# Kernel optimization log

Hardware: AMD Instinct MI355X
Metric: run time of the kernel (lower is better)

## Reference

```python
import jax, jax.numpy as jnp
import numpy as np

H = 768; NH = 12; HD = 64; LW = 256
NEG = -1e9  # finite stand-in for -inf; exp underflows to 0 identically in fp32 softmax

def setup_inputs() -> dict:
    key = jax.random.key(0)
    ks = jax.random.split(key, 10)
    s = 0.02
    return {
        "x": jax.random.normal(ks[0], (2, 2048, H), dtype=jnp.float32),
        "w_attn": jax.random.normal(ks[1], (H, 3 * H), dtype=jnp.float32) * s,
        "b_attn": jnp.zeros((3 * H,), dtype=jnp.float32),
        "w_proj": jax.random.normal(ks[2], (H, H), dtype=jnp.float32) * s,
        "b_proj": jnp.zeros((H,), dtype=jnp.float32),
        "w_sel1": jax.random.normal(ks[3], (H, H // 4), dtype=jnp.float32) * s,
        "b_sel1": jnp.zeros((H // 4,), dtype=jnp.float32),
        "w_sel2": jax.random.normal(ks[4], (H // 4, 1), dtype=jnp.float32) * s,
        "b_sel2": jnp.zeros((1,), dtype=jnp.float32),
        "local_weight": jnp.float32(0.5),
        "global_weight": jnp.float32(0.5),
    }

def reference(x, w_attn, b_attn, w_proj, b_proj, w_sel1, b_sel1, w_sel2, b_sel2,
              local_weight, global_weight):
    B, T, C = x.shape
    scale = HD ** -0.5
    qkv = x @ w_attn + b_attn                       # [B,T,3C]
    q, k, v = jnp.split(qkv, 3, axis=-1)
    q = q.reshape(B, T, NH, HD).transpose(0, 2, 1, 3)  # [B,H,T,D]
    k = k.reshape(B, T, NH, HD).transpose(0, 2, 1, 3)
    v = v.reshape(B, T, NH, HD).transpose(0, 2, 1, 3)
    scores = jnp.einsum('bhqd,bhkd->bhqk', q, k) * scale  # [B,H,T,T]
    i = jnp.arange(T)[:, None]
    j = jnp.arange(T)[None, :]
    causal = j > i
    scores = jnp.where(causal[None, None], NEG, scores)
    # selectivity: per-key-position gate in [0.2, 1.0]
    sel = jax.nn.sigmoid(jax.nn.gelu(x @ w_sel1 + b_sel1, approximate=False) @ w_sel2 + b_sel2)  # [B,T,1]
    sel = sel[:, None, :, 0][:, :, None, :]            # [B,1,1,T]
    modulated = scores * (0.2 + 0.8 * sel)
    outside_local = j < jnp.clip(i - LW, 0, None)
    local = jnp.where(outside_local[None, None], NEG, scores)
    wl = jax.nn.sigmoid(local_weight)
    wg = jax.nn.sigmoid(global_weight)
    wsum = wl + wg
    wl, wg = wl / wsum, wg / wsum
    attn = wl * jax.nn.softmax(local, axis=-1) + wg * jax.nn.softmax(modulated, axis=-1)
    out = jnp.einsum('bhqk,bhkd->bhqd', attn, v)        # [B,H,T,D]
    out = out.transpose(0, 2, 1, 3).reshape(B, T, C)
    return out @ w_proj + b_proj
```

## Files before the change

kernel.cpp:

```cpp
#include <hip/hip_runtime.h>
#include <cmath>

#define TT    2048
#define CC    768
#define NHEAD 12
#define LWIN  256
#define BBATCH 2
#define MROWS 4096
#define QBA   128
#define KB    64
#define NSLOT 72
#define L2E   1.4426950408889634f

typedef unsigned int u32;
typedef u32 u32x2 __attribute__((ext_vector_type(2)));
typedef u32 u32x4 __attribute__((ext_vector_type(4)));
typedef short bf16x8 __attribute__((ext_vector_type(8)));
typedef float f32x16 __attribute__((ext_vector_type(16)));

union F4 { u32x4 u; bf16x8 h; };

__device__ __forceinline__ unsigned short b16(float a) {
  u32 u = __float_as_uint(a);
  return (unsigned short)((u + 0x7FFFu + ((u >> 16) & 1u)) >> 16);
}
__device__ __forceinline__ u32 pk2(float a, float b) {
  return (u32)b16(a) | ((u32)b16(b) << 16);
}

__global__ __launch_bounds__(256) void cvt_bf16_kernel(
    const float* __restrict__ in, unsigned short* __restrict__ out, int n8) {
  const int i = blockIdx.x * 256 + threadIdx.x;
  if (i >= n8) return;
  const float4 a = *(const float4*)&in[(size_t)i * 8];
  const float4 b = *(const float4*)&in[(size_t)i * 8 + 4];
  u32x4 w = {pk2(a.x, a.y), pk2(a.z, a.w), pk2(b.x, b.y), pk2(b.z, b.w)};
  *(u32x4*)&out[(size_t)i * 8] = w;
}

__global__ __launch_bounds__(256) void transpose_cvt_kernel(
    const float* __restrict__ W, unsigned short* __restrict__ Wt, int K, int N) {
  __shared__ float t[32][33];
  const int tid = threadIdx.x;
  const int n0 = blockIdx.x * 32, k0 = blockIdx.y * 32;
  const int r = tid >> 5, c = tid & 31;
#pragma unroll
  for (int rr = 0; rr < 4; ++rr)
    t[r + 8 * rr][c] = W[(size_t)(k0 + r + 8 * rr) * N + n0 + c];
  __syncthreads();
#pragma unroll
  for (int rr = 0; rr < 4; ++rr)
    Wt[(size_t)(n0 + r + 8 * rr) * K + k0 + c] = b16(t[c][r + 8 * rr]);
}

template <int NT, bool OUTBF, int ACT>
__global__ __launch_bounds__(256) void gemm_mfma_kernel(
    const unsigned short* __restrict__ A, const unsigned short* __restrict__ Bt,
    const float* __restrict__ bias, void* __restrict__ Cout,
    int M, int N, int K) {
  __shared__ alignas(16) unsigned short as_[128 * 64];
  __shared__ alignas(16) unsigned short bs_[NT * 32 * 64];
  const int tid = threadIdx.x;
  const int lane = tid & 63;
  const int wv = tid >> 6;
  const int hi = lane >> 5;
  const int l31 = lane & 31;
  const int m0 = blockIdx.y * 128, n0 = blockIdx.x * (NT * 32);

  u32x4 ar[4], br[NT];

#define G_ISSUE(K0)                                                           \
  do {                                                                        \
    _Pragma("unroll") for (int i = 0; i < 4; ++i) {                           \
      const int idx = tid + (i << 8);                                         \
      const int r = idx >> 3, c = idx & 7;                                    \
      ar[i] = *(const u32x4*)&A[(size_t)(m0 + r) * K + (K0) + c * 8];         \
    }                                                                         \
    _Pragma("unroll") for (int i = 0; i < NT; ++i) {                          \
      const int idx = tid + (i << 8);                                         \
      const int r = idx >> 3, c = idx & 7;                                    \
      br[i] = *(const u32x4*)&Bt[(size_t)(n0 + r) * K + (K0) + c * 8];        \
    }                                                                         \
  } while (0)

#define G_WRITE()                                                             \
  do {                                                                        \
    _Pragma("unroll") for (int i = 0; i < 4; ++i) {                           \
      const int idx = tid + (i << 8);                                         \
      const int r = idx >> 3, c = idx & 7;                                    \
      *(u32x4*)((char*)as_ + r * 128 + ((c ^ (r & 7)) << 4)) = ar[i];         \
    }                                                                         \
    _Pragma("unroll") for (int i = 0; i < NT; ++i) {                          \
      const int idx = tid + (i << 8);                                         \
      const int r = idx >> 3, c = idx & 7;                                    \
      *(u32x4*)((char*)bs_ + r * 128 + ((c ^ (r & 7)) << 4)) = br[i];         \
    }                                                                         \
  } while (0)

  f32x16 acc[NT];
#pragma unroll
  for (int nt = 0; nt < NT; ++nt)
#pragma unroll
    for (int r = 0; r < 16; ++r) acc[nt][r] = 0.f;

  G_ISSUE(0);
  G_WRITE();
  __syncthreads();

  const int arow = wv * 32 + l31;
  for (int k0 = 0; k0 < K; k0 += 64) {
    if (k0 + 64 < K) G_ISSUE(k0 + 64);
#pragma unroll
    for (int s = 0; s < 4; ++s) {
      F4 af;
      af.u = *(const u32x4*)((const char*)as_ + arow * 128 +
                             (((2 * s + hi) ^ (arow & 7)) << 4));
#pragma unroll
      for (int nt = 0; nt < NT; ++nt) {
        F4 bf;
        bf.u = *(const u32x4*)((const char*)bs_ + (nt * 32 + l31) * 128 +
                               (((2 * s + hi) ^ (l31 & 7)) << 4));
        acc[nt] = __builtin_amdgcn_mfma_f32_32x32x16_bf16(af.h, bf.h, acc[nt], 0, 0, 0);
      }
    }
    __syncthreads();
    if (k0 + 64 < K) G_WRITE();
    __syncthreads();
  }

#pragma unroll
  for (int nt = 0; nt < NT; ++nt)
#pragma unroll
    for (int r = 0; r < 16; ++r) {
      const int m = m0 + wv * 32 + (r & 3) + 8 * (r >> 2) + 4 * hi;
      const int n = n0 + nt * 32 + l31;
      float v = acc[nt][r] + bias[n];
      if (ACT == 1) v = 0.5f * v * (1.f + erff(v * 0.70710678118654752f));
      if (OUTBF)
        ((unsigned short*)Cout)[(size_t)m * N + n] = b16(v);
      else
        ((float*)Cout)[(size_t)m * N + n] = v;
    }
#undef G_ISSUE
#undef G_WRITE
}

__global__ __launch_bounds__(256) void gate_kernel(
    const float* __restrict__ gh, const float* __restrict__ w2,
    const float* __restrict__ b2, float* __restrict__ gate) {
  const int lane = threadIdx.x & 63;
  const int row = blockIdx.x * 4 + (threadIdx.x >> 6);
  float s = 0.f;
#pragma unroll
  for (int j = 0; j < 3; ++j) {
    const int c = lane + 64 * j;
    s = fmaf(gh[(size_t)row * 192 + c], w2[c], s);
  }
#pragma unroll
  for (int off = 32; off; off >>= 1) s += __shfl_xor(s, off, 64);
  if (lane == 0) {
    const float sel = 1.f / (1.f + __expf(-(s + b2[0])));
    gate[row] = 0.125f * L2E * (0.2f + 0.8f * sel);
  }
}

__global__ __launch_bounds__(256) void attn_part_kernel(
    const unsigned short* __restrict__ qkvb, const float* __restrict__ gate8,
    unsigned short* __restrict__ part1O, unsigned short* __restrict__ part2O,
    float* __restrict__ part2ML) {
  __shared__ alignas(16) unsigned short k_s[2][KB * 64];
  __shared__ alignas(16) unsigned short vt_s[2][64 * 68];
  __shared__ float g_s[2][KB];

  const int tid = threadIdx.x;
  const int lane = tid & 63;
  const int wv = tid >> 6;
  const int hi = lane >> 5;
  const int l31 = lane & 31;
  const int bh = blockIdx.y;
  const int bb = bh / NHEAD;
  const int hh = bh % NHEAD;

  u32x4 kr[2], vr[2];
  float gr = 0.f;

#define A_ISSUE(T0, WG)                                                        \
  do {                                                                         \
    _Pragma("unroll") for (int i = 0; i < 2; ++i) {                            \
      const int idx = tid + (i << 8);                                          \
      const int r = idx >> 3, c = idx & 7;                                     \
      const size_t base = (size_t)(bb * TT + (T0) + r) * 2304 + hh * 64 + c * 8; \
      kr[i] = *(const u32x4*)&qkvb[base + 768];                                \
      vr[i] = *(const u32x4*)&qkvb[base + 1536];                               \
    }                                                                          \
    if (WG && tid < KB) gr = gate8[bb * TT + (T0) + tid];                      \
  } while (0)

#define A_WRITE(KD, VD, GD, WG)                                                \
  do {                                                                         \
    _Pragma("unroll") for (int i = 0; i < 2; ++i) {                            \
      const int idx = tid + (i << 8);                                          \
      const int r = idx >> 3, c = idx & 7;                                     \
      *(u32x4*)((char*)(KD) + r * 128 + ((c ^ (r & 7)) << 4)) = kr[i];         \
      const int d0 = c * 8;                                                    \
      (VD)[(d0 + 0) * 68 + r] = (unsigned short)(vr[i].x & 0xffff);            \
      (VD)[(d0 + 1) * 68 + r] = (unsigned short)(vr[i].x >> 16);               \
      (VD)[(d0 + 2) * 68 + r] = (unsigned short)(vr[i].y & 0xffff);            \
      (VD)[(d0 + 3) * 68 + r] = (unsigned short)(vr[i].y >> 16);               \
      (VD)[(d0 + 4) * 68 + r] = (unsigned short)(vr[i].z & 0xffff);            \
      (VD)[(d0 + 5) * 68 + r] = (unsigned short)(vr[i].z >> 16);               \
      (VD)[(d0 + 6) * 68 + r] = (unsigned short)(vr[i].w & 0xffff);            \
      (VD)[(d0 + 7) * 68 + r] = (unsigned short)(vr[i].w >> 16);               \
    }                                                                          \
    if (WG && tid < KB) (GD)[tid] = gr;                                        \
  } while (0)

#define QK_MFMA(KC)                                                            \
  do {                                                                         \
    _Pragma("unroll") for (int s = 0; s < 4; ++s) {                            \
      const int blk = (2 * s + hi) ^ (l31 & 7);                                \
      F4 f0, f1;                                                               \
      f0.u = *(const u32x4*)((const char*)(KC) + l31 * 128 + (blk << 4));      \
      f1.u = *(const u32x4*)((const char*)(KC) + (32 + l31) * 128 + (blk << 4));\
      S0 = __builtin_amdgcn_mfma_f32_32x32x16_bf16(f0.h, qf[s], S0, 0, 0, 0);  \
      S1 = __builtin_amdgcn_mfma_f32_32x32x16_bf16(f1.h, qf[s], S1, 0, 0, 0);  \
    }                                                                          \
  } while (0)

#define V_FRAGS(VC)                                                            \
  do {                                                                         \
    const char* vb0 = (const char*)(VC) + (size_t)l31 * 136 + hi * 8;          \
    const char* vb1 = vb0 + 32 * 136;                                          \
    _Pragma("unroll") for (int kb4 = 0; kb4 < 4; ++kb4) {                      \
      const u32x2 a0 = *(const u32x2*)(vb0 + 32 * kb4);                        \
      const u32x2 a1 = *(const u32x2*)(vb0 + 32 * kb4 + 16);                   \
      va[kb4].u = (u32x4){a0.x, a0.y, a1.x, a1.y};                             \
      const u32x2 c0 = *(const u32x2*)(vb1 + 32 * kb4);                        \
      const u32x2 c1 = *(const u32x2*)(vb1 + 32 * kb4 + 16);                   \
      vbf[kb4].u = (u32x4){c0.x, c0.y, c1.x, c1.y};                            \
    }                                                                          \
  } while (0)

#define SOFTMAX_PV(M, L, OA, OB)                                               \
  do {                                                                         \
    float red[8];                                                              \
    _Pragma("unroll") for (int i = 0; i < 8; ++i)                              \
      red[i] = fmaxf(fmaxf(S0[i], S0[i + 8]), fmaxf(S1[i], S1[i + 8]));        \
    _Pragma("unroll") for (int off = 4; off; off >>= 1)                        \
      _Pragma("unroll") for (int i = 0; i < off; ++i)                          \
        red[i] = fmaxf(red[i], red[i + off]);                                  \
    const float pmax = fmaxf(red[0], __shfl_xor(red[0], 32));                  \
    const int resc = __any(pmax > M + 8.f);                                    \
    float f = 1.f;                                                             \
    if (resc) {                                                                \
      const float mn = fmaxf(M, pmax);                                         \
      f = exp2f(M - mn);                                                       \
      M = mn;                                                                  \
    }                                                                          \
    _Pragma("unroll") for (int r = 0; r < 16; ++r) {                           \
      S0[r] = exp2f(S0[r] - M);                                                \
      S1[r] = exp2f(S1[r] - M);                                                \
    }                                                                          \
    _Pragma("unroll") for (int i = 0; i < 8; ++i)                              \
      red[i] = (S0[i] + S0[i + 8]) + (S1[i] + S1[i + 8]);                      \
    _Pragma("unroll") for (int off = 4; off; off >>= 1)                        \
      _Pragma("unroll") for (int i = 0; i < off; ++i)                          \
        red[i] += red[i + off];                                                \
    const float sum = red[0] + __shfl_xor(red[0], 32);                         \
    if (resc) {                                                                \
      L = L * f + sum;                                                         \
      _Pragma("unroll") for (int r = 0; r < 16; ++r) {                         \
        const float fq = __shfl(f, (r & 3) + 8 * (r >> 2) + 4 * hi);           \
        OA[r] *= fq;                                                           \
        OB[r] *= fq;                                                           \
      }                                                                        \
    } else {                                                                   \
      L += sum;                                                                \
    }                                                                          \
    u32 Pp[16];                                                                \
    _Pragma("unroll") for (int w = 0; w < 8; ++w) {                            \
      asm("v_cvt_pk_bf16_f32 %0, %1, %2" : "=v"(Pp[w]) : "v"(S0[2 * w]), "v"(S0[2 * w + 1])); \
      asm("v_cvt_pk_bf16_f32 %0, %1, %2" : "=v"(Pp[8 + w]) : "v"(S1[2 * w]), "v"(S1[2 * w + 1])); \
    }                                                                          \
    _Pragma("unroll") for (int kb4 = 0; kb4 < 4; ++kb4) {                      \
      F4 a;                                                                    \
      a.u = (u32x4){Pp[4 * kb4 + 0], Pp[4 * kb4 + 1], Pp[4 * kb4 + 2],         \
                    Pp[4 * kb4 + 3]};                                          \
      OA = __builtin_amdgcn_mfma_f32_32x32x16_bf16(a.h, va[kb4].h, OA, 0, 0, 0);\
      OB = __builtin_amdgcn_mfma_f32_32x32x16_bf16(a.h, vbf[kb4].h, OB, 0, 0, 0);\
    }                                                                          \
  } while (0)

  if (blockIdx.x >= 16) {
    const int slot = (NSLOT - 1) - (blockIdx.x - 16);
    const int g = (slot < 2) ? 0 : (slot < 6) ? 1 : (slot < 12) ? 2 :
                  (slot < 20) ? 3 : (slot < 30) ? 4 : (slot < 42) ? 5 :
                  (slot < 56) ? 6 : 7;
    const int idxg = slot - g * (g + 1);
    const int e = (idxg >= g + 1) ? 1 : 0;
    const int qt = 2 * g + e;
    const int ch = idxg - e * (g + 1);
    const int r0 = qt * QBA;
    const int r0w = r0 + wv * 32;
    const int iq = r0w + l31;
    const int tlo = ch * 4;
    const int thi = min(tlo + 4, 2 * (qt + 1));

    bf16x8 qf[4];
    {
      const size_t qrow = (size_t)(bb * TT + r0w + l31) * 2304 + hh * 64;
#pragma unroll
      for (int s = 0; s < 4; ++s) {
        F4 f;
        f.u = *(const u32x4*)&qkvb[qrow + 16 * s + 8 * hi];
        qf[s] = f.h;
      }
    }

    float m2 = -1e30f, l2 = 0.f;
    f32x16 O2a, O2b;
#pragma unroll
    for (int r = 0; r < 16; ++r) { O2a[r] = 0.f; O2b[r] = 0.f; }

    A_ISSUE(tlo * 64, 1);
    A_WRITE(k_s[0], vt_s[0], g_s[0], 1);
    __syncthreads();

    int cur = 0;
    for (int t = tlo; t < thi; ++t) {
      const int t0 = t << 6;
      if (t + 1 < thi) A_ISSUE((t + 1) * 64, 1);
      if (t0 <= r0w + 31) {
        f32x16 S0, S1;
#pragma unroll
        for (int r = 0; r < 16; ++r) { S0[r] = 0.f; S1[r] = 0.f; }
        QK_MFMA(k_s[cur]);
        F4 va[4], vbf[4];
        V_FRAGS(vt_s[cur]);
        if (t0 + 63 <= r0w) {
#pragma unroll
          for (int r = 0; r < 16; ++r) {
            const int crow = (r & 3) + 8 * (r >> 2) + 4 * hi;
            S0[r] *= g_s[cur][crow];
            S1[r] *= g_s[cur][32 + crow];
          }
        } else {
#pragma unroll
          for (int r = 0; r < 16; ++r) {
            const int crow = (r & 3) + 8 * (r >> 2) + 4 * hi;
            const int k0 = t0 + crow;
            S0[r] = (k0 <= iq) ? S0[r] * g_s[cur][crow] : -1e30f;
            S1[r] = (k0 + 32 <= iq) ? S1[r] * g_s[cur][32 + crow] : -1e30f;
          }
        }
        SOFTMAX_PV(m2, l2, O2a, O2b);
      }
      if (t + 1 < thi) A_WRITE(k_s[cur ^ 1], vt_s[cur ^ 1], g_s[cur ^ 1], 1);
      __syncthreads();
      cur ^= 1;
    }

    const size_t srow = ((size_t)bh * NSLOT + slot) * 128 + wv * 32;
    if (hi == 0) {
      float2 ml;
      ml.x = m2;
      ml.y = l2;
      *(float2*)&part2ML[(srow + l31) * 2] = ml;
    }
#pragma unroll
    for (int r = 0; r < 16; ++r) {
      const int crow = (r & 3) + 8 * (r >> 2) + 4 * hi;
      const size_t rowi = srow + crow;
      part2O[rowi * 64 + l31]      = b16(O2a[r]);
      part2O[rowi * 64 + 32 + l31] = b16(O2b[r]);
    }
  } else {
    const int qt = blockIdx.x;
    const int r0 = qt * QBA;
    const int r0w = r0 + wv * 32;
    const int iq = r0w + l31;
    int tlo = (r0 - LWIN) >> 6;
    tlo = tlo < 0 ? 0 : tlo;
    const int thi = (r0 + QBA) >> 6;

    bf16x8 qf[4];
    {
      const size_t qrow = (size_t)(bb * TT + r0w + l31) * 2304 + hh * 64;
#pragma unroll
      for (int s = 0; s < 4; ++s) {
        F4 f;
        f.u = *(const u32x4*)&qkvb[qrow + 16 * s + 8 * hi];
        qf[s] = f.h;
      }
    }

    float m1 = -1e30f, l1 = 0.f;
    f32x16 O1a, O1b;
#pragma unroll
    for (int r = 0; r < 16; ++r) { O1a[r] = 0.f; O1b[r] = 0.f; }

    A_ISSUE(tlo * 64, 0);
    A_WRITE(k_s[0], vt_s[0], g_s[0], 0);
    __syncthreads();

    int cur = 0;
    for (int t = tlo; t < thi; ++t) {
      const int t0 = t << 6;
      if (t + 1 < thi) A_ISSUE((t + 1) * 64, 0);
      if (t0 + 63 >= r0w - LWIN && t0 <= r0w + 31) {
        f32x16 S0, S1;
#pragma unroll
        for (int r = 0; r < 16; ++r) { S0[r] = 0.f; S1[r] = 0.f; }
        QK_MFMA(k_s[cur]);
        F4 va[4], vbf[4];
        V_FRAGS(vt_s[cur]);
        if (t0 + 63 <= r0w && t0 >= r0w + 31 - LWIN) {
#pragma unroll
          for (int r = 0; r < 16; ++r) {
            S0[r] *= (0.125f * L2E);
            S1[r] *= (0.125f * L2E);
          }
        } else {
#pragma unroll
          for (int r = 0; r < 16; ++r) {
            const int crow = (r & 3) + 8 * (r >> 2) + 4 * hi;
            const int k0 = t0 + crow;
            const bool ok0 = (k0 <= iq) && (k0 + LWIN >= iq);
            const bool ok1 = (k0 + 32 <= iq) && (k0 + 32 + LWIN >= iq);
            S0[r] = ok0 ? S0[r] * (0.125f * L2E) : -1e30f;
            S1[r] = ok1 ? S1[r] * (0.125f * L2E) : -1e30f;
          }
        }
        SOFTMAX_PV(m1, l1, O1a, O1b);
      }
      if (t + 1 < thi) A_WRITE(k_s[cur ^ 1], vt_s[cur ^ 1], g_s[cur ^ 1], 0);
      __syncthreads();
      cur ^= 1;
    }

    const size_t obase = (((size_t)bh * 16 + qt) * 128 + wv * 32) * 64;
#pragma unroll
    for (int r = 0; r < 16; ++r) {
      const int crow = (r & 3) + 8 * (r >> 2) + 4 * hi;
      const float inv = 1.f / __shfl(l1, crow);
      part1O[obase + (size_t)crow * 64 + l31]      = b16(O1a[r] * inv);
      part1O[obase + (size_t)crow * 64 + 32 + l31] = b16(O1b[r] * inv);
    }
  }
#undef A_ISSUE
#undef A_WRITE
#undef QK_MFMA
#undef V_FRAGS
#undef SOFTMAX_PV
}

__global__ __launch_bounds__(256) void combine_kernel(
    const unsigned short* __restrict__ part1O,
    const unsigned short* __restrict__ part2O,
    const float* __restrict__ part2ML,
    const float* __restrict__ lwp, const float* __restrict__ gwp,
    unsigned short* __restrict__ aob) {
  const int t = blockIdx.x * 256 + threadIdx.x;
  const int d8 = t & 7;
  const int rr = t >> 3;
  const int bh = rr >> 11;
  const int qrow = rr & 2047;
  const int qt = qrow >> 7, row = qrow & 127;
  const int g = qt >> 1;
  const int sb = g * (g + 1) + (qt & 1) * (g + 1);
  const int nc = g + 1;

  float m = -1e30f, l = 0.f;
  float oa[4], ob[4];
#pragma unroll
  for (int j = 0; j < 4; ++j) { oa[j] = 0.f; ob[j] = 0.f; }

  for (int c = 0; c < nc; ++c) {
    const size_t rowi = ((size_t)bh * NSLOT + sb + c) * 128 + row;
    const float2 ml = *(const float2*)&part2ML[rowi * 2];
    const u32x4 po = *(const u32x4*)&part2O[(rowi << 6) + 8 * d8];
    const float mn = fmaxf(m, ml.x);
    const float e0 = exp2f(m - mn), e1 = exp2f(ml.x - mn);
    l = l * e0 + ml.y * e1;
#pragma unroll
    for (int j = 0; j < 4; ++j) {
      oa[j] = oa[j] * e0 + __uint_as_float(po[j] << 16) * e1;
      ob[j] = ob[j] * e0 + __uint_as_float(po[j] & 0xffff0000u) * e1;
    }
    m = mn;
  }
  const u32x4 o1p = *(const u32x4*)&part1O[((((size_t)bh * 16 + qt) * 128 + row) << 6) + 8 * d8];
  const float wlr = 1.f / (1.f + __expf(-lwp[0]));
  const float wgr = 1.f / (1.f + __expf(-gwp[0]));
  const float wl = wlr / (wlr + wgr);
  const float wg = wgr / (wlr + wgr);
  const float s2 = wg / l;
  u32x4 outw;
#pragma unroll
  for (int j = 0; j < 4; ++j) {
    const float outa = wl * __uint_as_float(o1p[j] << 16) + oa[j] * s2;
    const float outb = wl * __uint_as_float(o1p[j] & 0xffff0000u) + ob[j] * s2;
    outw[j] = pk2(outa, outb);
  }
  const int bb = bh / NHEAD, hh = bh % NHEAD;
  *(u32x4*)&aob[(size_t)(bb * TT + qrow) * CC + hh * 64 + 8 * d8] = outw;
}

extern "C" void kernel_launch(void* const* d_in, const int* in_sizes, int n_in,
                              void* d_out, int out_size, void* d_ws, size_t ws_size,
                              hipStream_t stream) {
  const float* x      = (const float*)d_in[0];
  const float* w_attn = (const float*)d_in[1];
  const float* b_attn = (const float*)d_in[2];
  const float* w_proj = (const float*)d_in[3];
  const float* b_proj = (const float*)d_in[4];
  const float* w_sel1 = (const float*)d_in[5];
  const float* b_sel1 = (const float*)d_in[6];
  const float* w_sel2 = (const float*)d_in[7];
  const float* b_sel2 = (const float*)d_in[8];
  const float* lw     = (const float*)d_in[9];
  const float* gw     = (const float*)d_in[10];
  float* out = (float*)d_out;

  unsigned short* qkvb  = (unsigned short*)d_ws;
  unsigned short* xb    = qkvb + (size_t)MROWS * 2304;
  unsigned short* wta   = xb + (size_t)MROWS * 768;
  unsigned short* wtp   = wta + (size_t)2304 * 768;
  unsigned short* wts   = wtp + (size_t)768 * 768;
  unsigned short* aob   = wts + (size_t)192 * 768;
  unsigned short* part1O = aob + (size_t)MROWS * 768;
  unsigned short* part2O = part1O + (size_t)24 * 16 * 128 * 64;
  float* gatebuf = (float*)(part2O + (size_t)24 * NSLOT * 128 * 64);
  float* part2ML = gatebuf + MROWS;
  float* ghbuf   = part2ML + (size_t)24 * NSLOT * 128 * 2;

  cvt_bf16_kernel<<<(MROWS * 768 / 8 + 255) / 256, 256, 0, stream>>>(
      x, xb, MROWS * 768 / 8);
  transpose_cvt_kernel<<<dim3(2304 / 32, 768 / 32), 256, 0, stream>>>(
      w_attn, wta, 768, 2304);
  transpose_cvt_kernel<<<dim3(768 / 32, 768 / 32), 256, 0, stream>>>(
      w_proj, wtp, 768, 768);
  transpose_cvt_kernel<<<dim3(192 / 32, 768 / 32), 256, 0, stream>>>(
      w_sel1, wts, 768, 192);
  gemm_mfma_kernel<2, false, 1><<<dim3(192 / 64, MROWS / 128), 256, 0, stream>>>(
      xb, wts, b_sel1, ghbuf, MROWS, 192, 768);
  gate_kernel<<<MROWS / 4, 256, 0, stream>>>(ghbuf, w_sel2, b_sel2, gatebuf);
  gemm_mfma_kernel<4, true, 0><<<dim3(2304 / 128, MROWS / 128), 256, 0, stream>>>(
      xb, wta, b_attn, qkvb, MROWS, 2304, 768);
  attn_part_kernel<<<dim3(NSLOT + 16, BBATCH * NHEAD), 256, 0, stream>>>(
      qkvb, gatebuf, part1O, part2O, part2ML);
  combine_kernel<<<(BBATCH * NHEAD * TT * 8) / 256, 256, 0, stream>>>(
      part1O, part2O, part2ML, lw, gw, aob);
  gemm_mfma_kernel<2, false, 0><<<dim3(768 / 64, MROWS / 128), 256, 0, stream>>>(
      aob, wtp, b_proj, out, MROWS, 768, 768);
}
```

Baseline: 141.9 us.

## Load GEMM tiles and attention K tiles directly to LDS via global_load_lds

The GEMM kernel drops its register-staged double-buffered prefetch and instead issues global_load_lds (direct global-to-LDS) loads with an XOR swizzle, followed by a barrier before the MFMA loop. This removes VGPR staging and the separate LDS write pass. The attention kernel likewise moves K tiles to direct-to-LDS loads into the alternate buffer while V keeps its transposing register path. It also wraps the MFMA sections in s_setprio to favour matrix issue. The GEMM loses its overlap of the next tile's loads with compute, so each iteration now waits on load latency.

Measured after the change: 148.4 us. 1.05x slower.

```diff
diff --git a/kernel.cpp b/kernel.cpp
--- a/kernel.cpp
+++ b/kernel.cpp
@@ -26,6 +26,12 @@
 }
 __device__ __forceinline__ u32 pk2(float a, float b) {
   return (u32)b16(a) | ((u32)b16(b) << 16);
+}
+
+__device__ __forceinline__ void gll16(const unsigned short* g, unsigned short* l) {
+  __builtin_amdgcn_global_load_lds(
+      (const __attribute__((address_space(1))) void*)g,
+      (__attribute__((address_space(3))) void*)l, 16, 0, 0);
 }
 
 __global__ __launch_bounds__(256) void cvt_bf16_kernel(
@@ -67,49 +73,28 @@
   const int l31 = lane & 31;
   const int m0 = blockIdx.y * 128, n0 = blockIdx.x * (NT * 32);
 
-  u32x4 ar[4], br[NT];
-
-#define G_ISSUE(K0)                                                           \
-  do {                                                                        \
-    _Pragma("unroll") for (int i = 0; i < 4; ++i) {                           \
-      const int idx = tid + (i << 8);                                         \
-      const int r = idx >> 3, c = idx & 7;                                    \
-      ar[i] = *(const u32x4*)&A[(size_t)(m0 + r) * K + (K0) + c * 8];         \
-    }                                                                         \
-    _Pragma("unroll") for (int i = 0; i < NT; ++i) {                          \
-      const int idx = tid + (i << 8);                                         \
-      const int r = idx >> 3, c = idx & 7;                                    \
-      br[i] = *(const u32x4*)&Bt[(size_t)(n0 + r) * K + (K0) + c * 8];        \
-    }                                                                         \
-  } while (0)
-
-#define G_WRITE()                                                             \
-  do {                                                                        \
-    _Pragma("unroll") for (int i = 0; i < 4; ++i) {                           \
-      const int idx = tid + (i << 8);                                         \
-      const int r = idx >> 3, c = idx & 7;                                    \
-      *(u32x4*)((char*)as_ + r * 128 + ((c ^ (r & 7)) << 4)) = ar[i];         \
-    }                                                                         \
-    _Pragma("unroll") for (int i = 0; i < NT; ++i) {                          \
-      const int idx = tid + (i << 8);                                         \
-      const int r = idx >> 3, c = idx & 7;                                    \
-      *(u32x4*)((char*)bs_ + r * 128 + ((c ^ (r & 7)) << 4)) = br[i];         \
-    }                                                                         \
-  } while (0)
+  const int lrow = lane >> 3;
+  const int swz = ((lane & 7) ^ lrow) * 8;
 
   f32x16 acc[NT];
 #pragma unroll
   for (int nt = 0; nt < NT; ++nt)
 #pragma unroll
     for (int r = 0; r < 16; ++r) acc[nt][r] = 0.f;
-
-  G_ISSUE(0);
-  G_WRITE();
-  __syncthreads();
 
   const int arow = wv * 32 + l31;
   for (int k0 = 0; k0 < K; k0 += 64) {
-    if (k0 + 64 < K) G_ISSUE(k0 + 64);
+#pragma unroll
+    for (int i = 0; i < 4; ++i) {
+      const int j = wv * 4 + i;
+      gll16(&A[(size_t)(m0 + 8 * j + lrow) * K + k0 + swz], &as_[j * 512]);
+    }
+#pragma unroll
+    for (int i = 0; i < NT; ++i) {
+      const int j = wv * NT + i;
+      gll16(&Bt[(size_t)(n0 + 8 * j + lrow) * K + k0 + swz], &bs_[j * 512]);
+    }
+    __syncthreads();
 #pragma unroll
     for (int s = 0; s < 4; ++s) {
       F4 af;
@@ -123,8 +108,6 @@
         acc[nt] = __builtin_amdgcn_mfma_f32_32x32x16_bf16(af.h, bf.h, acc[nt], 0, 0, 0);
       }
     }
-    __syncthreads();
-    if (k0 + 64 < K) G_WRITE();
     __syncthreads();
   }
 
@@ -141,8 +124,6 @@
       else
         ((float*)Cout)[(size_t)m * N + n] = v;
     }
-#undef G_ISSUE
-#undef G_WRITE
 }
 
 __global__ __launch_bounds__(256) void gate_kernel(
@@ -177,31 +158,41 @@
   const int wv = tid >> 6;
   const int hi = lane >> 5;
   const int l31 = lane & 31;
+  const int lrow = lane >> 3;
+  const int swz = ((lane & 7) ^ lrow) * 8;
   const int bh = blockIdx.y;
   const int bb = bh / NHEAD;
   const int hh = bh % NHEAD;
 
-  u32x4 kr[2], vr[2];
+  u32x4 vr[2];
   float gr = 0.f;
 
-#define A_ISSUE(T0, WG)                                                        \
+#define K_GLL(T0, KD)                                                          \
+  do {                                                                         \
+    _Pragma("unroll") for (int i = 0; i < 2; ++i) {                            \
+      const int j = wv * 2 + i;                                                \
+      gll16(&qkvb[(size_t)(bb * TT + (T0) + 8 * j + lrow) * 2304 + hh * 64 +   \
+                  768 + swz],                                                  \
+            &(KD)[j * 512]);                                                   \
+    }                                                                          \
+  } while (0)
+
+#define V_ISSUE(T0, WG)                                                        \
   do {                                                                         \
     _Pragma("unroll") for (int i = 0; i < 2; ++i) {                            \
       const int idx = tid + (i << 8);                                          \
       const int r = idx >> 3, c = idx & 7;                                     \
-      const size_t base = (size_t)(bb * TT + (T0) + r) * 2304 + hh * 64 + c * 8; \
-      kr[i] = *(const u32x4*)&qkvb[base + 768];                                \
-      vr[i] = *(const u32x4*)&qkvb[base + 1536];                               \
+      vr[i] = *(const u32x4*)&qkvb[(size_t)(bb * TT + (T0) + r) * 2304 +       \
+                                   hh * 64 + 1536 + c * 8];                    \
     }                                                                          \
     if (WG && tid < KB) gr = gate8[bb * TT + (T0) + tid];                      \
   } while (0)
 
-#define A_WRITE(KD, VD, GD, WG)                                                \
+#define V_WRITE(VD, GD, WG)                                                    \
   do {                                                                         \
     _Pragma("unroll") for (int i = 0; i < 2; ++i) {                            \
       const int idx = tid + (i << 8);                                          \
       const int r = idx >> 3, c = idx & 7;                                     \
-      *(u32x4*)((char*)(KD) + r * 128 + ((c ^ (r & 7)) << 4)) = kr[i];         \
       const int d0 = c * 8;                                                    \
       (VD)[(d0 + 0) * 68 + r] = (unsigned short)(vr[i].x & 0xffff);            \
       (VD)[(d0 + 1) * 68 + r] = (unsigned short)(vr[i].x >> 16);               \
@@ -217,6 +208,7 @@
 
 #define QK_MFMA(KC)                                                            \
   do {                                                                         \
+    __builtin_amdgcn_s_setprio(1);                                             \
     _Pragma("unroll") for (int s = 0; s < 4; ++s) {                            \
       const int blk = (2 * s + hi) ^ (l31 & 7);                                \
       F4 f0, f1;                                                               \
@@ -225,6 +217,7 @@
       S0 = __builtin_amdgcn_mfma_f32_32x32x16_bf16(f0.h, qf[s], S0, 0, 0, 0);  \
       S1 = __builtin_amdgcn_mfma_f32_32x32x16_bf16(f1.h, qf[s], S1, 0, 0, 0);  \
     }                                                                          \
+    __builtin_amdgcn_s_setprio(0);                                             \
   } while (0)
 
 #define V_FRAGS(VC)                                                            \
@@ -282,6 +275,7 @@
       asm("v_cvt_pk_bf16_f32 %0, %1, %2" : "=v"(Pp[w]) : "v"(S0[2 * w]), "v"(S0[2 * w + 1])); \
       asm("v_cvt_pk_bf16_f32 %0, %1, %2" : "=v"(Pp[8 + w]) : "v"(S1[2 * w]), "v"(S1[2 * w + 1])); \
     }                                                                          \
+    __builtin_amdgcn_s_setprio(1);                                             \
     _Pragma("unroll") for (int kb4 = 0; kb4 < 4; ++kb4) {                      \
       F4 a;                                                                    \
       a.u = (u32x4){Pp[4 * kb4 + 0], Pp[4 * kb4 + 1], Pp[4 * kb4 + 2],         \
@@ -289,6 +283,7 @@
       OA = __builtin_amdgcn_mfma_f32_32x32x16_bf16(a.h, va[kb4].h, OA, 0, 0, 0);\
       OB = __builtin_amdgcn_mfma_f32_32x32x16_bf16(a.h, vbf[kb4].h, OB, 0, 0, 0);\
     }                                                                          \
+    __builtin_amdgcn_s_setprio(0);                                             \
   } while (0)
 
   if (blockIdx.x >= 16) {
@@ -322,14 +317,18 @@
 #pragma unroll
     for (int r = 0; r < 16; ++r) { O2a[r] = 0.f; O2b[r] = 0.f; }
 
-    A_ISSUE(tlo * 64, 1);
-    A_WRITE(k_s[0], vt_s[0], g_s[0], 1);
+    K_GLL(tlo * 64, k_s[0]);
+    V_ISSUE(tlo * 64, 1);
+    V_WRITE(vt_s[0], g_s[0], 1);
     __syncthreads();
 
     int cur = 0;
     for (int t = tlo; t < thi; ++t) {
       const int t0 = t << 6;
-      if (t + 1 < thi) A_ISSUE((t + 1) * 64, 1);
+      if (t + 1 < thi) {
+        K_GLL((t + 1) * 64, k_s[cur ^ 1]);
+        V_ISSUE((t + 1) * 64, 1);
+      }
       if (t0 <= r0w + 31) {
         f32x16 S0, S1;
 #pragma unroll
@@ -355,7 +354,7 @@
         }
         SOFTMAX_PV(m2, l2, O2a, O2b);
       }
-      if (t + 1 < thi) A_WRITE(k_s[cur ^ 1], vt_s[cur ^ 1], g_s[cur ^ 1], 1);
+      if (t + 1 < thi) V_WRITE(vt_s[cur ^ 1], g_s[cur ^ 1], 1);
       __syncthreads();
       cur ^= 1;
     }
@@ -399,14 +398,18 @@
 #pragma unroll
     for (int r = 0; r < 16; ++r) { O1a[r] = 0.f; O1b[r] = 0.f; }
 
-    A_ISSUE(tlo * 64, 0);
-    A_WRITE(k_s[0], vt_s[0], g_s[0], 0);
+    K_GLL(tlo * 64, k_s[0]);
+    V_ISSUE(tlo * 64, 0);
+    V_WRITE(vt_s[0], g_s[0], 0);
     __syncthreads();
 
     int cur = 0;
     for (int t = tlo; t < thi; ++t) {
       const int t0 = t << 6;
-      if (t + 1 < thi) A_ISSUE((t + 1) * 64, 0);
+      if (t + 1 < thi) {
+        K_GLL((t + 1) * 64, k_s[cur ^ 1]);
+        V_ISSUE((t + 1) * 64, 0);
+      }
       if (t0 + 63 >= r0w - LWIN && t0 <= r0w + 31) {
         f32x16 S0, S1;
 #pragma unroll
@@ -433,7 +436,7 @@
         }
         SOFTMAX_PV(m1, l1, O1a, O1b);
       }
-      if (t + 1 < thi) A_WRITE(k_s[cur ^ 1], vt_s[cur ^ 1], g_s[cur ^ 1], 0);
+      if (t + 1 < thi) V_WRITE(vt_s[cur ^ 1], g_s[cur ^ 1], 0);
       __syncthreads();
       cur ^= 1;
     }
@@ -447,8 +450,9 @@
       part1O[obase + (size_t)crow * 64 + 32 + l31] = b16(O1b[r] * inv);
     }
   }
-#undef A_ISSUE
-#undef A_WRITE
+#undef K_GLL
+#undef V_ISSUE
+#undef V_WRITE
 #undef QK_MFMA
 #undef V_FRAGS
 #undef SOFTMAX_PV
```
